# Performance work log

Measured on AMD Instinct MI355X. Metric: run time of the kernel, lower is better.

The kernel has to match this reference:

```python
import jax, jax.numpy as jnp
import numpy as np

N_NODES = 100000
N_EDGES = 1600000
N_FEAT = 128
HID = 64


def setup_inputs() -> dict:
    key = jax.random.key(0)
    ks = jax.random.split(key, 8)
    s = 0.05
    return {
        "x": jax.random.normal(ks[0], (N_NODES, N_FEAT), jnp.float32),
        "edge_index": jax.random.randint(ks[1], (2, N_EDGES), 0, N_NODES, jnp.int64),
        "labels": jax.random.randint(ks[2], (N_NODES, 1), 0, 2, jnp.int32),
        "W1": jax.random.normal(ks[3], (N_FEAT, HID), jnp.float32) * s,
        "b1": jnp.zeros((HID,), jnp.float32),
        "W2": jax.random.normal(ks[4], (HID, HID), jnp.float32) * s,
        "b2": jnp.zeros((HID,), jnp.float32),
        "W3": jax.random.normal(ks[5], (HID, HID), jnp.float32) * s,
        "b3": jnp.zeros((HID,), jnp.float32),
        "lW1": jax.random.normal(ks[6], (HID, 8), jnp.float32) * s,
        "lb1": jnp.zeros((8,), jnp.float32),
        "lW2": jax.random.normal(ks[7], (8, 1), jnp.float32) * s,
        "lb2": jnp.zeros((1,), jnp.float32),
    }


def reference(x, edge_index, labels, W1, b1, W2, b2, W3, b3, lW1, lb1, lW2, lb2):
    n = x.shape[0]
    # PyG GCNConv: add self-loops, symmetric D^{-1/2}(A+I)D^{-1/2} normalization
    loop = jnp.arange(n)
    row = jnp.concatenate([edge_index[0], loop])  # sources
    col = jnp.concatenate([edge_index[1], loop])  # targets (aggregation)
    deg = jax.ops.segment_sum(jnp.ones(col.shape, x.dtype), col, num_segments=n)
    dinv = jax.lax.rsqrt(deg)  # deg >= 1 thanks to self loops
    norm = dinv[row] * dinv[col]  # [E+N]

    def gcn(h, W, b):
        m = (h @ W)[row] * norm[:, None]  # gather + scale per edge
        return jax.ops.segment_sum(m, col, num_segments=n) + b

    h = jax.nn.relu(gcn(x, W1, b1))   # dropout inactive in eval mode
    h = jax.nn.relu(gcn(h, W2, b2))
    h = jax.nn.relu(gcn(h, W3, b3))
    h = jax.nn.relu(h @ lW1 + lb1)
    p = jax.nn.sigmoid(h @ lW2 + lb2)  # [N,1]

    y = labels.astype(x.dtype)
    # generate_weights(labels): class-balance weights (minority class up-weighted)
    pm = jnp.mean(y)
    w = y * (1.0 - pm) + (1.0 - y) * pm
    eps = 1e-7
    pc = jnp.clip(p, eps, 1.0 - eps)
    bce = -(y * jnp.log(pc) + (1.0 - y) * jnp.log(1.0 - pc))
    loss = jnp.mean(w * bce)
    return loss, p
```

## Files before the change

kernel.cpp:

```cpp
#include <hip/hip_runtime.h>
#include <cstdint>
#include <cstddef>

typedef __attribute__((ext_vector_type(8))) short short8;
typedef __attribute__((ext_vector_type(4))) float f32x4;
typedef __attribute__((ext_vector_type(2))) float f32x2;

#define NBLK 512
#define NBLK_SHIFT 9

__device__ inline unsigned short f2bf(float f) {
  union { float f; unsigned int u; } x; x.f = f;
  unsigned int r = x.u + 0x7FFFu + ((x.u >> 16) & 1u);
  return (unsigned short)(r >> 16);
}
__device__ inline float bf2f(unsigned short s) {
  union { unsigned int u; float f; } x; x.u = ((unsigned int)s) << 16;
  return x.f;
}


__global__ __launch_bounds__(256) void hist_kernel(const int* __restrict__ cols,
                                                   int* __restrict__ histG,
                                                   const int* __restrict__ labels,
                                                   float* __restrict__ labelsum,
                                                   const float* __restrict__ W1,
                                                   const float* __restrict__ W2,
                                                   const float* __restrict__ W3,
                                                   unsigned short* __restrict__ Wt1,
                                                   unsigned short* __restrict__ Wt2,
                                                   unsigned short* __restrict__ Wt3,
                                                   unsigned char* __restrict__ zrow_a,
                                                   unsigned char* __restrict__ zrow_b,
                                                   int E, int N, int NBUCK) {
  __shared__ int h[512];
  if (blockIdx.x < 3) {
    const float* W; unsigned short* Wt; int K;
    if (blockIdx.x == 0)      { W = W1; Wt = Wt1; K = 128; }
    else if (blockIdx.x == 1) { W = W2; Wt = Wt2; K = 64; }
    else                      { W = W3; Wt = Wt3; K = 64; }
    int total = K * 64;
    for (int i = threadIdx.x; i < total; i += 256) {
      int n = i / K, k = i - n * K;
      Wt[i] = f2bf(W[k * 64 + n]);
    }
  } else if (blockIdx.x == 3 && threadIdx.x < 32) {
    if (threadIdx.x < 16) ((unsigned int*)zrow_a)[threadIdx.x] = 0u;
    else                  ((unsigned int*)zrow_b)[threadIdx.x - 16] = 0u;
  }
  {
    int chunkL = (N + NBLK - 1) / NBLK;
    int ls = blockIdx.x * chunkL;
    int le = min(N, ls + chunkL);
    float v = 0.f;
    for (int i = ls + threadIdx.x; i < le; i += 256) v += (float)labels[i];
#pragma unroll
    for (int o = 32; o > 0; o >>= 1) v += __shfl_down(v, o);
    __shared__ float sl[4];
    if ((threadIdx.x & 63) == 0) sl[threadIdx.x >> 6] = v;
    __syncthreads();
    if (threadIdx.x == 0) labelsum[blockIdx.x] = sl[0] + sl[1] + sl[2] + sl[3];
  }
  for (int i = threadIdx.x; i < NBUCK; i += 256) h[i] = 0;
  __syncthreads();
  int chunk = (E + NBLK - 1) / NBLK;
  int s = blockIdx.x * chunk;
  int e = min(E, s + chunk);
  for (int i = s + threadIdx.x; i < e; i += 256) atomicAdd(&h[cols[i] >> 8], 1);
  __syncthreads();
  for (int i = threadIdx.x; i < NBUCK; i += 256)
    histG[blockIdx.x * NBUCK + i] = h[i];
}


__global__ __launch_bounds__(256) void scan_partials_t(const int* __restrict__ histG,
                                                       int* __restrict__ partials,
                                                       int total, int NBUCK) {
  int i = blockIdx.x * 256 + threadIdx.x;
  int v = 0;
  if (i < total) {
    int bucket = i >> NBLK_SHIFT, blk = i & (NBLK - 1);
    v = histG[blk * NBUCK + bucket];
  }
#pragma unroll
  for (int o = 32; o > 0; o >>= 1) v += __shfl_down(v, o);
  __shared__ int s[4];
  if ((threadIdx.x & 63) == 0) s[threadIdx.x >> 6] = v;
  __syncthreads();
  if (threadIdx.x == 0) partials[blockIdx.x] = s[0] + s[1] + s[2] + s[3];
}

__global__ __launch_bounds__(256) void scan_block(int* __restrict__ partials, int nb,
                                                  float* __restrict__ loss,
                                                  const float* __restrict__ labelsum,
                                                  float* __restrict__ pmsum) {
  __shared__ int tmp[256];
  __shared__ int carry;
  int tid = threadIdx.x;
  {
    float v = 0.f;
    for (int i = tid; i < NBLK; i += 256) v += labelsum[i];
#pragma unroll
    for (int o = 32; o > 0; o >>= 1) v += __shfl_down(v, o);
    __shared__ float sl[4];
    if ((tid & 63) == 0) sl[tid >> 6] = v;
    __syncthreads();
    if (tid == 0) *pmsum = sl[0] + sl[1] + sl[2] + sl[3];
  }
  if (tid == 0) { carry = 0; *loss = 0.f; }
  __syncthreads();
  for (int base = 0; base < nb; base += 256) {
    int i = base + tid;
    int v = (i < nb) ? partials[i] : 0;
    tmp[tid] = v;
    __syncthreads();
    int incl = v;
    for (int o = 1; o < 256; o <<= 1) {
      int t = (tid >= o) ? tmp[tid - o] : 0;
      __syncthreads();
      incl += t;
      tmp[tid] = incl;
      __syncthreads();
    }
    int total = tmp[255];
    int c = carry;
    if (i < nb) partials[i] = c + incl - v;
    __syncthreads();
    if (tid == 0) carry = c + total;
    __syncthreads();
  }
}

__global__ __launch_bounds__(256) void scan_final_t(const int* __restrict__ histG,
                                                    const int* __restrict__ partials,
                                                    int* __restrict__ scannedG,
                                                    int total, int NBUCK) {
  __shared__ int tmp[256];
  int tid = threadIdx.x;
  int i = blockIdx.x * 256 + tid;
  int bucket = i >> NBLK_SHIFT, blk = i & (NBLK - 1);
  int v = (i < total) ? histG[blk * NBUCK + bucket] : 0;
  tmp[tid] = v;
  __syncthreads();
  int incl = v;
  for (int o = 1; o < 256; o <<= 1) {
    int t = (tid >= o) ? tmp[tid - o] : 0;
    __syncthreads();
    incl += t;
    tmp[tid] = incl;
    __syncthreads();
  }
  if (i < total) scannedG[blk * NBUCK + bucket] = partials[blockIdx.x] + incl - v;
}


__global__ __launch_bounds__(256) void scatter_kernel(const int* __restrict__ rows,
                                                      const int* __restrict__ cols,
                                                      const int* __restrict__ scannedG,
                                                      unsigned int* __restrict__ packed,
                                                      int E, int NBUCK) {
  __shared__ int cur[512];
  for (int i = threadIdx.x; i < NBUCK; i += 256)
    cur[i] = scannedG[blockIdx.x * NBUCK + i];
  __syncthreads();
  int chunk = (E + NBLK - 1) / NBLK;
  int s = blockIdx.x * chunk;
  int e = min(E, s + chunk);
  for (int i = s + threadIdx.x; i < e; i += 256) {
    int c = cols[i];
    int r = rows[i];
    int pos = atomicAdd(&cur[c >> 8], 1);
    packed[pos] = ((unsigned int)(c & 255) << 24) | (unsigned int)r;
  }
}


__global__ __launch_bounds__(1024) void csr_finalize(const unsigned int* __restrict__ packed,
                                                     const int* __restrict__ scannedG,
                                                     int* __restrict__ sorted_src,
                                                     int* __restrict__ offsets,
                                                     float* __restrict__ dinv,
                                                     int N, int E, int NBUCK) {
  __shared__ int h[256];
  __shared__ int tmp[256];
  __shared__ int cur[256];
  int b = blockIdx.x;
  int tid = threadIdx.x;
  int base = scannedG[b];
  int end = (b + 1 < NBUCK) ? scannedG[b + 1] : E;
  if (tid < 256) h[tid] = 0;
  __syncthreads();
  for (int i = base + tid; i < end; i += 1024)
    atomicAdd(&h[packed[i] >> 24], 1);
  __syncthreads();
  if (tid < 256) {
    int v = h[tid];
    tmp[tid] = v;
  }
  __syncthreads();
  if (tid < 256) {
    int v = h[tid];
    int incl = v;
    for (int o = 1; o < 256; o <<= 1) {
      int t = (tid >= o) ? tmp[tid - o] : 0;
      __syncthreads();
      incl += t;
      tmp[tid] = incl;
      __syncthreads();
    }
    int excl = incl - v;
    int node = b * 256 + tid;
    if (node < N) {
      offsets[node] = base + excl;
      dinv[node] = rsqrtf((float)(v + 1));
    }
    cur[tid] = base + excl;
    if (b == NBUCK - 1 && tid == 0) offsets[N] = E;
  } else {
    for (int o = 1; o < 256; o <<= 1) { __syncthreads(); __syncthreads(); }
  }
  __syncthreads();
  for (int i = base + tid; i < end; i += 1024) {
    unsigned int p = packed[i];
    int pos = atomicAdd(&cur[p >> 24], 1);
    sorted_src[pos] = (int)(p & 0xFFFFFFu);
  }
}


__global__ __launch_bounds__(256) void mfma_gemm1(const float* __restrict__ xv,
                                                  const unsigned short* __restrict__ Wt,
                                                  const float* __restrict__ dinv,
                                                  unsigned char* __restrict__ out, int N) {
  const int K = 128;
  __shared__ unsigned short tile[4][16 * 68];
  int w = threadIdx.x >> 6, lane = threadIdx.x & 63;
  int m = lane & 15, quad = lane >> 4;
  int m0 = blockIdx.x * 64 + w * 16;
  int rowA = m0 + m;
  bool rowOK = rowA < N;
  f32x4 acc[4] = {{0.f,0.f,0.f,0.f},{0.f,0.f,0.f,0.f},{0.f,0.f,0.f,0.f},{0.f,0.f,0.f,0.f}};
#pragma unroll
  for (int kc = 0; kc < K / 32; ++kc) {
    short8 a = {0, 0, 0, 0, 0, 0, 0, 0};
    if (rowOK) {
      const float* hp = xv + (size_t)rowA * K + kc * 32 + quad * 8;
      float4 p0 = ((const float4*)hp)[0];
      float4 p1 = ((const float4*)hp)[1];
      a[0] = (short)f2bf(p0.x); a[1] = (short)f2bf(p0.y);
      a[2] = (short)f2bf(p0.z); a[3] = (short)f2bf(p0.w);
      a[4] = (short)f2bf(p1.x); a[5] = (short)f2bf(p1.y);
      a[6] = (short)f2bf(p1.z); a[7] = (short)f2bf(p1.w);
    }
#pragma unroll
    for (int t = 0; t < 4; ++t) {
      short8 b = *(const short8*)(Wt + (size_t)(t * 16 + m) * K + kc * 32 + quad * 8);
      acc[t] = __builtin_amdgcn_mfma_f32_16x16x32_bf16(a, b, acc[t], 0, 0, 0);
    }
  }
  unsigned short* tw = tile[w];
#pragma unroll
  for (int r = 0; r < 4; ++r) {
    int row = quad * 4 + r;
    int gr = m0 + row;
    float dv = dinv[gr < N ? gr : 0];
#pragma unroll
    for (int t = 0; t < 4; ++t)
      tw[row * 68 + t * 16 + m] = f2bf(acc[t][r] * dv);
  }
#pragma unroll
  for (int p = 0; p < 4; ++p) {
    int row = p * 4 + (lane >> 4);
    int ch = lane & 15;
    int gr = m0 + row;
    if (gr < N) {
      uint2 v = *(const uint2*)(tw + row * 68 + ch * 4);
      float f0 = bf2f((unsigned short)(v.x & 0xFFFFu));
      float f1 = bf2f((unsigned short)(v.x >> 16));
      float f2 = bf2f((unsigned short)(v.y & 0xFFFFu));
      float f3 = bf2f((unsigned short)(v.y >> 16));
      int pk = 0;
      pk = __builtin_amdgcn_cvt_pk_fp8_f32(f0, f1, pk, false);
      pk = __builtin_amdgcn_cvt_pk_fp8_f32(f2, f3, pk, true);
      *(unsigned int*)(out + (size_t)gr * 64 + ch * 4) = (unsigned int)pk;
    }
  }
}


#define GATHER_CORE(A8in, ZR)                                                    \
  f32x2 a0={0.f,0.f},a1={0.f,0.f},a2={0.f,0.f},a3={0.f,0.f};                     \
  f32x2 a4={0.f,0.f},a5={0.f,0.f},a6={0.f,0.f},a7={0.f,0.f};                     \
  for (int base = s; base < e; base += 16) {                                     \
    int i0 = base + l4 * 4;                                                      \
    int r0 = (i0     < e) ? __builtin_nontemporal_load(sorted_src + i0)     : ZR;\
    int r1 = (i0 + 1 < e) ? __builtin_nontemporal_load(sorted_src + i0 + 1) : ZR;\
    int r2 = (i0 + 2 < e) ? __builtin_nontemporal_load(sorted_src + i0 + 2) : ZR;\
    int r3 = (i0 + 3 < e) ? __builtin_nontemporal_load(sorted_src + i0 + 3) : ZR;\
    int rj[16];                                                                  \
    _Pragma("unroll")                                                            \
    for (int s4 = 0; s4 < 4; ++s4) {                                             \
      rj[s4 * 4 + 0] = __shfl(r0, qbase + s4);                                   \
      rj[s4 * 4 + 1] = __shfl(r1, qbase + s4);                                   \
      rj[s4 * 4 + 2] = __shfl(r2, qbase + s4);                                   \
      rj[s4 * 4 + 3] = __shfl(r3, qbase + s4);                                   \
    }                                                                            \
    uint4 v[16];                                                                 \
    _Pragma("unroll")                                                            \
    for (int t = 0; t < 16; ++t)                                                 \
      v[t] = *(const uint4*)(A8in + ((size_t)(unsigned int)rj[t] << 6) + l4 * 16);\
    __builtin_amdgcn_sched_barrier(0);                                           \
    _Pragma("unroll")                                                            \
    for (int t = 0; t < 16; ++t) {                                               \
      a0 += __builtin_amdgcn_cvt_pk_f32_fp8((int)v[t].x, false);                 \
      a1 += __builtin_amdgcn_cvt_pk_f32_fp8((int)v[t].x, true);                  \
      a2 += __builtin_amdgcn_cvt_pk_f32_fp8((int)v[t].y, false);                 \
      a3 += __builtin_amdgcn_cvt_pk_f32_fp8((int)v[t].y, true);                  \
      a4 += __builtin_amdgcn_cvt_pk_f32_fp8((int)v[t].z, false);                 \
      a5 += __builtin_amdgcn_cvt_pk_f32_fp8((int)v[t].z, true);                  \
      a6 += __builtin_amdgcn_cvt_pk_f32_fp8((int)v[t].w, false);                 \
      a7 += __builtin_amdgcn_cvt_pk_f32_fp8((int)v[t].w, true);                  \
    }                                                                            \
  }


__global__ __launch_bounds__(256, 4) void agg_gemm(const unsigned char* __restrict__ A8in,
                                                   const int* __restrict__ offsets,
                                                   const int* __restrict__ sorted_src,
                                                   const float* __restrict__ dinv,
                                                   const float* __restrict__ bias,
                                                   const unsigned short* __restrict__ Wt,
                                                   unsigned char* __restrict__ A8out,
                                                   int N, int ZR) {
  __shared__ unsigned short hl[64 * 72];
  int lane = threadIdx.x & 63;
  int cl = threadIdx.x >> 2;
  int c = blockIdx.x * 64 + cl;
  int l4 = lane & 3;
  int qbase = lane & 60;
  bool ok = c < N;
  int s = 0, e = 0;
  float dc = 0.f;
  uint4 svr = {0u, 0u, 0u, 0u};
  if (ok) {
    s = offsets[c]; e = offsets[c + 1];
    dc = dinv[c];
    svr = *(const uint4*)(A8in + ((size_t)c << 6) + l4 * 16);
  }
  GATHER_CORE(A8in, ZR)
  {
    short8 w0 = {0,0,0,0,0,0,0,0}, w1 = {0,0,0,0,0,0,0,0};
    if (ok) {
      a0 += __builtin_amdgcn_cvt_pk_f32_fp8((int)svr.x, false);
      a1 += __builtin_amdgcn_cvt_pk_f32_fp8((int)svr.x, true);
      a2 += __builtin_amdgcn_cvt_pk_f32_fp8((int)svr.y, false);
      a3 += __builtin_amdgcn_cvt_pk_f32_fp8((int)svr.y, true);
      a4 += __builtin_amdgcn_cvt_pk_f32_fp8((int)svr.z, false);
      a5 += __builtin_amdgcn_cvt_pk_f32_fp8((int)svr.z, true);
      a6 += __builtin_amdgcn_cvt_pk_f32_fp8((int)svr.w, false);
      a7 += __builtin_amdgcn_cvt_pk_f32_fp8((int)svr.w, true);
      float accf[16] = {a0[0],a0[1],a1[0],a1[1],a2[0],a2[1],a3[0],a3[1],
                        a4[0],a4[1],a5[0],a5[1],a6[0],a6[1],a7[0],a7[1]};
      const float* bp = bias + l4 * 16;
#pragma unroll
      for (int q = 0; q < 8; ++q) {
        float v = fmaf(accf[q], dc, bp[q]);
        w0[q] = (short)f2bf(v > 0.f ? v : 0.f);
      }
#pragma unroll
      for (int q = 0; q < 8; ++q) {
        float v = fmaf(accf[8 + q], dc, bp[8 + q]);
        w1[q] = (short)f2bf(v > 0.f ? v : 0.f);
      }
    }
    short8* dst = (short8*)(hl + cl * 72 + l4 * 16);
    dst[0] = w0; dst[1] = w1;
  }
  __syncthreads();
  int wv = threadIdx.x >> 6;
  int m = lane & 15, quad = lane >> 4;
  int rbase = wv * 16;
  f32x4 acc2[4] = {{0.f,0.f,0.f,0.f},{0.f,0.f,0.f,0.f},{0.f,0.f,0.f,0.f},{0.f,0.f,0.f,0.f}};
#pragma unroll
  for (int kc = 0; kc < 2; ++kc) {
    short8 a = *(const short8*)(hl + (rbase + m) * 72 + kc * 32 + quad * 8);
#pragma unroll
    for (int t = 0; t < 4; ++t) {
      short8 b = *(const short8*)(Wt + (size_t)(t * 16 + m) * 64 + kc * 32 + quad * 8);
      acc2[t] = __builtin_amdgcn_mfma_f32_16x16x32_bf16(a, b, acc2[t], 0, 0, 0);
    }
  }
  __syncthreads();
#pragma unroll
  for (int r = 0; r < 4; ++r) {
    int row = rbase + quad * 4 + r;
    int gr = blockIdx.x * 64 + row;
    float dv = dinv[gr < N ? gr : 0];
#pragma unroll
    for (int t = 0; t < 4; ++t)
      hl[row * 72 + t * 16 + m] = f2bf(acc2[t][r] * dv);
  }
  __syncthreads();
#pragma unroll
  for (int u = 0; u < 4; ++u) {
    int id = u * 256 + threadIdx.x;
    int row = id >> 4, ch = id & 15;
    int gr = blockIdx.x * 64 + row;
    if (gr < N) {
      uint2 v = *(const uint2*)(hl + row * 72 + ch * 4);
      float f0 = bf2f((unsigned short)(v.x & 0xFFFFu));
      float f1 = bf2f((unsigned short)(v.x >> 16));
      float f2 = bf2f((unsigned short)(v.y & 0xFFFFu));
      float f3 = bf2f((unsigned short)(v.y >> 16));
      int pk = 0;
      pk = __builtin_amdgcn_cvt_pk_fp8_f32(f0, f1, pk, false);
      pk = __builtin_amdgcn_cvt_pk_fp8_f32(f2, f3, pk, true);
      *(unsigned int*)(A8out + (size_t)gr * 64 + ch * 4) = (unsigned int)pk;
    }
  }
}


__global__ __launch_bounds__(256, 4) void agg_head(const unsigned char* __restrict__ A8in,
                                                   const int* __restrict__ offsets,
                                                   const int* __restrict__ sorted_src,
                                                   const float* __restrict__ dinv,
                                                   const float* __restrict__ bias,
                                                   const float* __restrict__ lW1,
                                                   const float* __restrict__ lb1,
                                                   const float* __restrict__ lW2,
                                                   const float* __restrict__ lb2,
                                                   const int* __restrict__ labels,
                                                   const float* __restrict__ pmsum,
                                                   float* __restrict__ p,
                                                   float* __restrict__ loss,
                                                   int N, int ZR) {
  int lane = threadIdx.x & 63;
  int cl = threadIdx.x >> 2;
  int c = blockIdx.x * 64 + cl;
  int l4 = lane & 3;
  int qbase = lane & 60;
  bool ok = c < N;
  int s = 0, e = 0;
  float dc = 0.f;
  uint4 svr = {0u, 0u, 0u, 0u};
  if (ok) {
    s = offsets[c]; e = offsets[c + 1];
    dc = dinv[c];
    svr = *(const uint4*)(A8in + ((size_t)c << 6) + l4 * 16);
  }
  GATHER_CORE(A8in, ZR)
  float contrib = 0.f;
  {
    a0 += __builtin_amdgcn_cvt_pk_f32_fp8((int)svr.x, false);
    a1 += __builtin_amdgcn_cvt_pk_f32_fp8((int)svr.x, true);
    a2 += __builtin_amdgcn_cvt_pk_f32_fp8((int)svr.y, false);
    a3 += __builtin_amdgcn_cvt_pk_f32_fp8((int)svr.y, true);
    a4 += __builtin_amdgcn_cvt_pk_f32_fp8((int)svr.z, false);
    a5 += __builtin_amdgcn_cvt_pk_f32_fp8((int)svr.z, true);
    a6 += __builtin_amdgcn_cvt_pk_f32_fp8((int)svr.w, false);
    a7 += __builtin_amdgcn_cvt_pk_f32_fp8((int)svr.w, true);
    float accf[16] = {a0[0],a0[1],a1[0],a1[1],a2[0],a2[1],a3[0],a3[1],
                      a4[0],a4[1],a5[0],a5[1],a6[0],a6[1],a7[0],a7[1]};
    const float* bp = bias + l4 * 16;
    float hq[16];
#pragma unroll
    for (int q = 0; q < 16; ++q) {
      float v = fmaf(accf[q], dc, bp[q]);
      hq[q] = v > 0.f ? v : 0.f;
    }
    float acc8[8] = {0.f,0.f,0.f,0.f,0.f,0.f,0.f,0.f};
#pragma unroll
    for (int q = 0; q < 16; ++q) {
      int k = l4 * 16 + q;
#pragma unroll
      for (int j = 0; j < 8; ++j) acc8[j] = fmaf(hq[q], lW1[k * 8 + j], acc8[j]);
    }
#pragma unroll
    for (int j = 0; j < 8; ++j) {
      acc8[j] += __shfl_xor(acc8[j], 1);
      acc8[j] += __shfl_xor(acc8[j], 2);
    }
    if (ok && l4 == 0) {
      float sv = lb2[0];
#pragma unroll
      for (int j = 0; j < 8; ++j) {
        float a = acc8[j] + lb1[j];
        a = a > 0.f ? a : 0.f;
        sv = fmaf(a, lW2[j], sv);
      }
      float pv = 1.0f / (1.0f + expf(-sv));
      p[c] = pv;
      float pm = *pmsum / (float)N;
      float y = (float)labels[c];
      float w = y * (1.f - pm) + (1.f - y) * pm;
      float pc = fminf(fmaxf(pv, 1e-7f), 1.f - 1e-7f);
      float bce = -(y * logf(pc) + (1.f - y) * logf(1.f - pc));
      contrib = w * bce / (float)N;
    }
  }
#pragma unroll
  for (int o = 32; o > 0; o >>= 1) contrib += __shfl_down(contrib, o);
  __shared__ float sh[4];
  int wv = threadIdx.x >> 6;
  if (lane == 0) sh[wv] = contrib;
  __syncthreads();
  if (threadIdx.x == 0) atomicAdd(loss, sh[0] + sh[1] + sh[2] + sh[3]);
}


extern "C" void kernel_launch(void* const* d_in, const int* in_sizes, int n_in,
                              void* d_out, int out_size, void* d_ws, size_t ws_size,
                              hipStream_t stream) {
  const float* x      = (const float*)d_in[0];
  const int*   ei     = (const int*)d_in[1];
  const int*   labels = (const int*)d_in[2];
  const float* W1 = (const float*)d_in[3];
  const float* b1 = (const float*)d_in[4];
  const float* W2 = (const float*)d_in[5];
  const float* b2 = (const float*)d_in[6];
  const float* W3 = (const float*)d_in[7];
  const float* b3 = (const float*)d_in[8];
  const float* lW1 = (const float*)d_in[9];
  const float* lb1 = (const float*)d_in[10];
  const float* lW2 = (const float*)d_in[11];
  const float* lb2 = (const float*)d_in[12];

  int N = in_sizes[2];
  int E = in_sizes[1] / 2;
  const int* rows = ei;
  const int* cols = ei + E;

  int Npad = (N + 63) & ~63;
  int NBUCK = (N + 255) >> 8;
  int totalH = NBUCK * NBLK;
  int nb2 = (totalH + 255) / 256;

  size_t a8stride = (size_t)Npad * 64 + 256;
  char* ws = (char*)d_ws;
  unsigned char*  A8a = (unsigned char*)ws;
  unsigned char*  A8b = (unsigned char*)(ws + a8stride);
  unsigned short* Wt1 = (unsigned short*)(ws + (size_t)Npad * 192);
  unsigned short* Wt2 = Wt1 + 64 * 128;
  unsigned short* Wt3 = Wt2 + 64 * 64;
  float* dinv     = (float*)(Wt3 + 64 * 64);
  int*   offsets  = (int*)(dinv + N);
  int*   histG    = offsets + N + 1;
  int*   scanned  = histG + totalH;
  unsigned int* packed = (unsigned int*)(scanned + totalH);
  int*   sorted   = (int*)(packed + E);
  int*   partials = sorted + E;
  float* pmsum    = (float*)(partials + nb2);
  float* labelsum = pmsum + 1;

  float* loss = (float*)d_out;
  float* p    = (float*)d_out + 1;

  int gemmBlocks = Npad / 64;
  int aggBlocks  = (N + 63) / 64;
  int ZR = Npad;

  hist_kernel<<<NBLK, 256, 0, stream>>>(cols, histG, labels, labelsum,
                                        W1, W2, W3, Wt1, Wt2, Wt3,
                                        A8a + (size_t)Npad * 64, A8b + (size_t)Npad * 64,
                                        E, N, NBUCK);
  scan_partials_t<<<nb2, 256, 0, stream>>>(histG, partials, totalH, NBUCK);
  scan_block<<<1, 256, 0, stream>>>(partials, nb2, loss, labelsum, pmsum);
  scan_final_t<<<nb2, 256, 0, stream>>>(histG, partials, scanned, totalH, NBUCK);
  scatter_kernel<<<NBLK, 256, 0, stream>>>(rows, cols, scanned, packed, E, NBUCK);
  csr_finalize<<<NBUCK, 1024, 0, stream>>>(packed, scanned, sorted, offsets, dinv, N, E, NBUCK);

  mfma_gemm1<<<gemmBlocks, 256, 0, stream>>>(x, Wt1, dinv, A8a, N);

  agg_gemm<<<aggBlocks, 256, 0, stream>>>(A8a, offsets, sorted, dinv, b1, Wt2, A8b, N, ZR);
  agg_gemm<<<aggBlocks, 256, 0, stream>>>(A8b, offsets, sorted, dinv, b2, Wt3, A8a, N, ZR);
  agg_head<<<aggBlocks, 256, 0, stream>>>(A8a, offsets, sorted, dinv, b3,
                                          lW1, lb1, lW2, lb2, labels, pmsum, p, loss, N, ZR);
}
```

Baseline: 278.5 us.

## Fuse first GEMM into CSR finalize and swizzle block-to-chunk mapping

The first-layer bf16 MFMA GEMM now runs inside the CSR finalize kernel. Each 1024-thread block handles its own 256-node bucket and reads degree normalisation from shared memory instead of global dinv, which removes one launch and a dinv round trip. The histogram and scatter kernels also remap block IDs to edge chunks with an interleaving swizzle, likely to spread memory traffic across XCDs or channels. The fused kernel uses more shared memory (about 35 KB for the GEMM tiles) at 1024 threads, and the GEMM work now waits on each block's scatter phase, which may reduce occupancy.

```diff
diff --git a/kernel.cpp b/kernel.cpp
--- a/kernel.cpp
+++ b/kernel.cpp
@@ -8,6 +8,8 @@
 
 #define NBLK 512
 #define NBLK_SHIFT 9
+
+__device__ inline int chunk_of_block(int bid) { return ((bid & 7) << 6) | (bid >> 3); }
 
 __device__ inline unsigned short f2bf(float f) {
   union { float f; unsigned int u; } x; x.f = f;
@@ -63,13 +65,14 @@
   }
   for (int i = threadIdx.x; i < NBUCK; i += 256) h[i] = 0;
   __syncthreads();
+  int cchunk = chunk_of_block(blockIdx.x);
   int chunk = (E + NBLK - 1) / NBLK;
-  int s = blockIdx.x * chunk;
+  int s = cchunk * chunk;
   int e = min(E, s + chunk);
   for (int i = s + threadIdx.x; i < e; i += 256) atomicAdd(&h[cols[i] >> 8], 1);
   __syncthreads();
   for (int i = threadIdx.x; i < NBUCK; i += 256)
-    histG[blockIdx.x * NBUCK + i] = h[i];
+    histG[cchunk * NBUCK + i] = h[i];
 }
 
 
@@ -160,11 +163,12 @@
                                                       unsigned int* __restrict__ packed,
                                                       int E, int NBUCK) {
   __shared__ int cur[512];
+  int cchunk = chunk_of_block(blockIdx.x);
   for (int i = threadIdx.x; i < NBUCK; i += 256)
-    cur[i] = scannedG[blockIdx.x * NBUCK + i];
+    cur[i] = scannedG[cchunk * NBUCK + i];
   __syncthreads();
   int chunk = (E + NBLK - 1) / NBLK;
-  int s = blockIdx.x * chunk;
+  int s = cchunk * chunk;
   int e = min(E, s + chunk);
   for (int i = s + threadIdx.x; i < e; i += 256) {
     int c = cols[i];
@@ -175,15 +179,20 @@
 }
 
 
-__global__ __launch_bounds__(1024) void csr_finalize(const unsigned int* __restrict__ packed,
-                                                     const int* __restrict__ scannedG,
-                                                     int* __restrict__ sorted_src,
-                                                     int* __restrict__ offsets,
-                                                     float* __restrict__ dinv,
-                                                     int N, int E, int NBUCK) {
+__global__ __launch_bounds__(1024) void csr_finalize_gemm1(const unsigned int* __restrict__ packed,
+                                                           const int* __restrict__ scannedG,
+                                                           int* __restrict__ sorted_src,
+                                                           int* __restrict__ offsets,
+                                                           float* __restrict__ dinv,
+                                                           const float* __restrict__ xv,
+                                                           const unsigned short* __restrict__ Wt,
+                                                           unsigned char* __restrict__ out,
+                                                           int N, int E, int NBUCK) {
   __shared__ int h[256];
   __shared__ int tmp[256];
   __shared__ int cur[256];
+  __shared__ float sdinv[256];
+  __shared__ unsigned short gtile[16][16 * 68];
   int b = blockIdx.x;
   int tid = threadIdx.x;
   int base = scannedG[b];
@@ -210,10 +219,12 @@
     }
     int excl = incl - v;
     int node = b * 256 + tid;
+    float dv = rsqrtf((float)(v + 1));
     if (node < N) {
       offsets[node] = base + excl;
-      dinv[node] = rsqrtf((float)(v + 1));
-    }
+      dinv[node] = dv;
+    }
+    sdinv[tid] = dv;
     cur[tid] = base + excl;
     if (b == NBUCK - 1 && tid == 0) offsets[N] = E;
   } else {
@@ -225,64 +236,59 @@
     int pos = atomicAdd(&cur[p >> 24], 1);
     sorted_src[pos] = (int)(p & 0xFFFFFFu);
   }
-}
-
-
-__global__ __launch_bounds__(256) void mfma_gemm1(const float* __restrict__ xv,
-                                                  const unsigned short* __restrict__ Wt,
-                                                  const float* __restrict__ dinv,
-                                                  unsigned char* __restrict__ out, int N) {
-  const int K = 128;
-  __shared__ unsigned short tile[4][16 * 68];
-  int w = threadIdx.x >> 6, lane = threadIdx.x & 63;
-  int m = lane & 15, quad = lane >> 4;
-  int m0 = blockIdx.x * 64 + w * 16;
-  int rowA = m0 + m;
-  bool rowOK = rowA < N;
-  f32x4 acc[4] = {{0.f,0.f,0.f,0.f},{0.f,0.f,0.f,0.f},{0.f,0.f,0.f,0.f},{0.f,0.f,0.f,0.f}};
-#pragma unroll
-  for (int kc = 0; kc < K / 32; ++kc) {
-    short8 a = {0, 0, 0, 0, 0, 0, 0, 0};
-    if (rowOK) {
-      const float* hp = xv + (size_t)rowA * K + kc * 32 + quad * 8;
-      float4 p0 = ((const float4*)hp)[0];
-      float4 p1 = ((const float4*)hp)[1];
-      a[0] = (short)f2bf(p0.x); a[1] = (short)f2bf(p0.y);
-      a[2] = (short)f2bf(p0.z); a[3] = (short)f2bf(p0.w);
-      a[4] = (short)f2bf(p1.x); a[5] = (short)f2bf(p1.y);
-      a[6] = (short)f2bf(p1.z); a[7] = (short)f2bf(p1.w);
-    }
-#pragma unroll
-    for (int t = 0; t < 4; ++t) {
-      short8 b = *(const short8*)(Wt + (size_t)(t * 16 + m) * K + kc * 32 + quad * 8);
-      acc[t] = __builtin_amdgcn_mfma_f32_16x16x32_bf16(a, b, acc[t], 0, 0, 0);
-    }
-  }
-  unsigned short* tw = tile[w];
-#pragma unroll
-  for (int r = 0; r < 4; ++r) {
-    int row = quad * 4 + r;
-    int gr = m0 + row;
-    float dv = dinv[gr < N ? gr : 0];
-#pragma unroll
-    for (int t = 0; t < 4; ++t)
-      tw[row * 68 + t * 16 + m] = f2bf(acc[t][r] * dv);
-  }
-#pragma unroll
-  for (int p = 0; p < 4; ++p) {
-    int row = p * 4 + (lane >> 4);
-    int ch = lane & 15;
-    int gr = m0 + row;
-    if (gr < N) {
-      uint2 v = *(const uint2*)(tw + row * 68 + ch * 4);
-      float f0 = bf2f((unsigned short)(v.x & 0xFFFFu));
-      float f1 = bf2f((unsigned short)(v.x >> 16));
-      float f2 = bf2f((unsigned short)(v.y & 0xFFFFu));
-      float f3 = bf2f((unsigned short)(v.y >> 16));
-      int pk = 0;
-      pk = __builtin_amdgcn_cvt_pk_fp8_f32(f0, f1, pk, false);
-      pk = __builtin_amdgcn_cvt_pk_fp8_f32(f2, f3, pk, true);
-      *(unsigned int*)(out + (size_t)gr * 64 + ch * 4) = (unsigned int)pk;
+  {
+    const int K = 128;
+    int wv = tid >> 6;
+    int lane = tid & 63;
+    int m = lane & 15, quad = lane >> 4;
+    int lrow0 = wv * 16;
+    int m0 = b * 256 + lrow0;
+    int rowA = m0 + m;
+    bool rowOK = rowA < N;
+    f32x4 acc[4] = {{0.f,0.f,0.f,0.f},{0.f,0.f,0.f,0.f},{0.f,0.f,0.f,0.f},{0.f,0.f,0.f,0.f}};
+#pragma unroll
+    for (int kc = 0; kc < K / 32; ++kc) {
+      short8 a = {0, 0, 0, 0, 0, 0, 0, 0};
+      if (rowOK) {
+        const float* hp = xv + (size_t)rowA * K + kc * 32 + quad * 8;
+        float4 p0 = ((const float4*)hp)[0];
+        float4 p1 = ((const float4*)hp)[1];
+        a[0] = (short)f2bf(p0.x); a[1] = (short)f2bf(p0.y);
+        a[2] = (short)f2bf(p0.z); a[3] = (short)f2bf(p0.w);
+        a[4] = (short)f2bf(p1.x); a[5] = (short)f2bf(p1.y);
+        a[6] = (short)f2bf(p1.z); a[7] = (short)f2bf(p1.w);
+      }
+#pragma unroll
+      for (int t = 0; t < 4; ++t) {
+        short8 bb = *(const short8*)(Wt + (size_t)(t * 16 + m) * K + kc * 32 + quad * 8);
+        acc[t] = __builtin_amdgcn_mfma_f32_16x16x32_bf16(a, bb, acc[t], 0, 0, 0);
+      }
+    }
+    unsigned short* tw = gtile[wv];
+#pragma unroll
+    for (int r = 0; r < 4; ++r) {
+      int row = quad * 4 + r;
+      float dv = sdinv[lrow0 + row];
+#pragma unroll
+      for (int t = 0; t < 4; ++t)
+        tw[row * 68 + t * 16 + m] = f2bf(acc[t][r] * dv);
+    }
+#pragma unroll
+    for (int p = 0; p < 4; ++p) {
+      int row = p * 4 + (lane >> 4);
+      int ch = lane & 15;
+      int gr = m0 + row;
+      if (gr < N) {
+        uint2 v = *(const uint2*)(tw + row * 68 + ch * 4);
+        float f0 = bf2f((unsigned short)(v.x & 0xFFFFu));
+        float f1 = bf2f((unsigned short)(v.x >> 16));
+        float f2 = bf2f((unsigned short)(v.y & 0xFFFFu));
+        float f3 = bf2f((unsigned short)(v.y >> 16));
+        int pk = 0;
+        pk = __builtin_amdgcn_cvt_pk_fp8_f32(f0, f1, pk, false);
+        pk = __builtin_amdgcn_cvt_pk_fp8_f32(f2, f3, pk, true);
+        *(unsigned int*)(out + (size_t)gr * 64 + ch * 4) = (unsigned int)pk;
+      }
     }
   }
 }
@@ -556,7 +562,6 @@
   float* loss = (float*)d_out;
   float* p    = (float*)d_out + 1;
 
-  int gemmBlocks = Npad / 64;
   int aggBlocks  = (N + 63) / 64;
   int ZR = Npad;
 
@@ -568,9 +573,9 @@
   scan_block<<<1, 256, 0, stream>>>(partials, nb2, loss, labelsum, pmsum);
   scan_final_t<<<nb2, 256, 0, stream>>>(histG, partials, scanned, totalH, NBUCK);
   scatter_kernel<<<NBLK, 256, 0, stream>>>(rows, cols, scanned, packed, E, NBUCK);
-  csr_finalize<<<NBUCK, 1024, 0, stream>>>(packed, scanned, sorted, offsets, dinv, N, E, NBUCK);
-
-  mfma_gemm1<<<gemmBlocks, 256, 0, stream>>>(x, Wt1, dinv, A8a, N);
+
+  csr_finalize_gemm1<<<NBUCK, 1024, 0, stream>>>(packed, scanned, sorted, offsets, dinv,
+                                                 x, Wt1, A8a, N, E, NBUCK);
 
   agg_gemm<<<aggBlocks, 256, 0, stream>>>(A8a, offsets, sorted, dinv, b1, Wt2, A8b, N, ZR);
   agg_gemm<<<aggBlocks, 256, 0, stream>>>(A8b, offsets, sorted, dinv, b2, Wt3, A8a, N, ZR);
```

Result: no change. 278.9 us (median of 2 runs) (+0.2%).
